# Performance work log

Hardware: AMD Instinct MI355X
Metric: run time of the kernel (lower is better)

## Reference

```python
import jax, jax.numpy as jnp
import numpy as np

B, C_IN, H, W = 8, 32, 64, 64
C = 64  # num_channels


def setup_inputs() -> dict:
    key = jax.random.key(0)
    ks = jax.random.split(key, 9)
    s_in = 1.0 / np.sqrt(C_IN)
    s_c = 1.0 / np.sqrt(C)
    return {
        "x": jax.random.normal(ks[0], (B, C_IN, H, W), dtype=jnp.float32),
        "wq": jax.random.uniform(ks[1], (C, C_IN), jnp.float32, -s_in, s_in),
        "bq": jax.random.uniform(ks[2], (C,), jnp.float32, -s_in, s_in),
        "wk": jax.random.uniform(ks[3], (C, C_IN), jnp.float32, -s_in, s_in),
        "bk": jax.random.uniform(ks[4], (C,), jnp.float32, -s_in, s_in),
        "wv": jax.random.uniform(ks[5], (C, C_IN), jnp.float32, -s_in, s_in),
        "bv": jax.random.uniform(ks[6], (C,), jnp.float32, -s_in, s_in),
        "wo": jax.random.uniform(ks[7], (C_IN, C), jnp.float32, -s_c, s_c),
        "bo": jax.random.uniform(ks[8], (C_IN,), jnp.float32, -s_c, s_c),
    }


def reference(x, wq, bq, wk, bk, wv, bv, wo, bo):
    b, c_in, h, w = x.shape
    n = h * w
    # 1x1 convs == per-pixel linear projections; produce (B, N, C) directly
    q = (jnp.einsum('bchw,oc->bhwo', x, wq) + bq).reshape(b, n, -1)
    k = (jnp.einsum('bchw,oc->bhwo', x, wk) + bk).reshape(b, n, -1)
    v = (jnp.einsum('bchw,oc->bhwo', x, wv) + bv).reshape(b, n, -1)
    # unscaled attention over spatial positions (no 1/sqrt(d) in original)
    scores = jnp.einsum('bnc,bmc->bnm', q, k)  # (B, N, N)
    attn = jax.nn.softmax(scores, axis=-1)
    out = jnp.einsum('bnm,bmc->bnc', attn, v)  # (B, N, C)
    out = out.reshape(b, h, w, -1)
    out = jnp.einsum('bhwc,oc->bohw', out, wo) + bo[None, :, None, None]
    return out + x
```

## Files before the change

kernel.cpp:

```cpp
#include <hip/hip_runtime.h>
#include <hip/hip_bf16.h>

#define CIN    32
#define NPIX   4096
#define DIM    64
#define LOG2E  1.4426950408889634f

#if __has_builtin(__builtin_amdgcn_exp2f)
#define EXP2(x) __builtin_amdgcn_exp2f(x)
#else
#define EXP2(x) exp2f(x)
#endif

typedef float  f32x4  __attribute__((ext_vector_type(4)));
typedef float  f32x16 __attribute__((ext_vector_type(16)));
typedef short  s16x8  __attribute__((ext_vector_type(8)));

#define ZERO16 {0.f,0.f,0.f,0.f,0.f,0.f,0.f,0.f,0.f,0.f,0.f,0.f,0.f,0.f,0.f,0.f}

__device__ __forceinline__ f32x16 mfma32(s16x8 a, s16x8 b, f32x16 c) {
    return __builtin_amdgcn_mfma_f32_32x32x16_bf16(a, b, c, 0, 0, 0);
}


__global__ __launch_bounds__(256) void qkv_proj(
    const float* __restrict__ x,
    const float* __restrict__ wq, const float* __restrict__ bq,
    const float* __restrict__ wk, const float* __restrict__ bk,
    const float* __restrict__ wv, const float* __restrict__ bv,
    __hip_bfloat16* __restrict__ qb, __hip_bfloat16* __restrict__ kb,
    __hip_bfloat16* __restrict__ vb)
{
    __shared__ float Xs[CIN][64];
    __shared__ float wT[3][CIN][DIM];

    const int tid = threadIdx.x;
    const int b   = blockIdx.y;
    const int bx  = blockIdx.x;
    const int n0  = bx * 64;

    for (int i = tid; i < 3 * CIN * DIM; i += 256) {
        int m = i >> 11, r = i & 2047, c = r >> 6, o = r & 63;
        const float* wsrc = (m == 0) ? wq : (m == 1) ? wk : wv;
        float wv0 = wsrc[o * CIN + c];
        wT[m][c][o] = (m == 0) ? wv0 * LOG2E : wv0;
    }
    for (int i = tid * 4; i < CIN * 64; i += 1024) {
        int c = i >> 6, p = i & 63;
        *(f32x4*)&Xs[c][p] = *(const f32x4*)&x[((size_t)b * CIN + c) * NPIX + n0 + p];
    }
    __syncthreads();

    const int w    = tid >> 6;
    const int lane = tid & 63;
    const int l16  = lane >> 2;
    const int quad = lane & 3;

    const int T  = bx * 4 + w;
    const int px = T * 16 + l16;

    float aq[2][8], ak[2][8];
    #pragma unroll
    for (int kb2 = 0; kb2 < 2; kb2++) {
        f32x4 bq0 = *(const f32x4*)&bq[kb2 * 32 + quad * 8];
        f32x4 bq1 = *(const f32x4*)&bq[kb2 * 32 + quad * 8 + 4];
        f32x4 bk0 = *(const f32x4*)&bk[kb2 * 32 + quad * 8];
        f32x4 bk1 = *(const f32x4*)&bk[kb2 * 32 + quad * 8 + 4];
        #pragma unroll
        for (int j = 0; j < 4; j++) {
            aq[kb2][j] = bq0[j] * LOG2E; aq[kb2][j + 4] = bq1[j] * LOG2E;
            ak[kb2][j] = bk0[j];         ak[kb2][j + 4] = bk1[j];
        }
    }
    #pragma unroll 8
    for (int c = 0; c < CIN; c++) {
        const float xc = Xs[c][w * 16 + l16];
        #pragma unroll
        for (int kb2 = 0; kb2 < 2; kb2++) {
            f32x4 q0 = *(const f32x4*)&wT[0][c][kb2 * 32 + quad * 8];
            f32x4 q1 = *(const f32x4*)&wT[0][c][kb2 * 32 + quad * 8 + 4];
            f32x4 k0 = *(const f32x4*)&wT[1][c][kb2 * 32 + quad * 8];
            f32x4 k1 = *(const f32x4*)&wT[1][c][kb2 * 32 + quad * 8 + 4];
            #pragma unroll
            for (int j = 0; j < 4; j++) {
                aq[kb2][j]     += xc * q0[j];
                aq[kb2][j + 4] += xc * q1[j];
                ak[kb2][j]     += xc * k0[j];
                ak[kb2][j + 4] += xc * k1[j];
            }
        }
    }
    {
        const int s   = px >> 5;
        const int key = px & 31;
        #pragma unroll
        for (int kb2 = 0; kb2 < 2; kb2++) {
            union { s16x8 v; __hip_bfloat16 h[8]; } pq, pk;
            #pragma unroll
            for (int j = 0; j < 8; j++) {
                pq.h[j] = __float2bfloat16(aq[kb2][j]);
                pk.h[j] = __float2bfloat16(ak[kb2][j]);
            }
            *(s16x8*)(qb + ((size_t)b * NPIX + px) * DIM + kb2 * 32 + quad * 8) = pq.v;
            const int kt = kb2 * 2 + (quad >> 1);
            const int h  = quad & 1;
            const size_t koff = (size_t)b * 262144
                + ((size_t)(s * 4 + kt) * 64 + h * 32 + key) * 8;
            *(s16x8*)(kb + koff) = pk.v;
        }
    }

    const int ch = w * 16 + l16;
    float av[2][8];
    {
        const float bvc = bv[ch];
        #pragma unroll
        for (int kh = 0; kh < 2; kh++)
            #pragma unroll
            for (int j = 0; j < 8; j++) av[kh][j] = bvc;
    }
    #pragma unroll 8
    for (int c = 0; c < CIN; c++) {
        const float wvc = wT[2][c][ch];
        f32x4 x0 = *(const f32x4*)&Xs[c][quad * 8];
        f32x4 x1 = *(const f32x4*)&Xs[c][quad * 8 + 4];
        f32x4 x2 = *(const f32x4*)&Xs[c][32 + quad * 8];
        f32x4 x3 = *(const f32x4*)&Xs[c][32 + quad * 8 + 4];
        #pragma unroll
        for (int j = 0; j < 4; j++) {
            av[0][j]     += x0[j] * wvc;
            av[0][j + 4] += x1[j] * wvc;
            av[1][j]     += x2[j] * wvc;
            av[1][j + 4] += x3[j] * wvc;
        }
    }
    #pragma unroll
    for (int kh = 0; kh < 2; kh++) {
        const int s = bx * 2 + kh;
        #pragma unroll
        for (int h = 0; h < 2; h++) {
            union { unsigned long long u; __hip_bfloat16 hh[4]; } pv;
            #pragma unroll
            for (int j = 0; j < 4; j++) pv.hh[j] = __float2bfloat16(av[kh][h * 4 + j]);
            const size_t voff = (size_t)b * 262144
                + (size_t)(s * 4 + (ch >> 5) * 2 + (quad >> 1)) * 512
                + (size_t)(h * 32 + (ch & 31)) * 8
                + 4 * (quad & 1);
            *(unsigned long long*)(vb + voff) = pv.u;
        }
    }
}

__global__ __launch_bounds__(512, 2) void attn_fused(
    const __hip_bfloat16* __restrict__ qb,
    const __hip_bfloat16* __restrict__ kbf,
    const __hip_bfloat16* __restrict__ vbf,
    const float* __restrict__ wo, const float* __restrict__ bo,
    const float* __restrict__ x, float* __restrict__ y)
{
    __shared__ __align__(16) char  sm[2][4][4096];
    __shared__ __align__(16) float REDx[4][64][33];
    __shared__ float LRED2[4][32];

    const int tid  = threadIdx.x;
    const int w    = tid >> 6;
    const int g    = w >> 1;
    const int h    = w & 1;
    const int lane = tid & 63;
    const int q    = lane & 31;
    const int hl   = lane >> 5;
    const int b    = blockIdx.x;
    const int row0 = blockIdx.y * 128 + g * 32;

    s16x8 qf[4];
    #pragma unroll
    for (int kt = 0; kt < 4; kt++)
        qf[kt] = *(const s16x8*)(qb + ((size_t)b * NPIX + row0 + q) * DIM
                                 + kt * 16 + hl * 8);

    f32x16 o0 = ZERO16, o1 = ZERO16;
    f32x16 ol = ZERO16;

    s16x8 ones8;
    #pragma unroll
    for (int j = 0; j < 8; j++) ones8[j] = (short)0x3F80;

    const char* stsrc = ((w & 4) ? (const char*)vbf : (const char*)kbf)
                        + (size_t)b * 524288
                        + (size_t)((w >> 1) & 1) * 262144
                        + (size_t)(w & 1) * 2048 + (size_t)lane * 16;
    char* std0 = &sm[0][w >> 1][(w & 1) * 2048 + lane * 16];
    char* std1 = std0 + 16384;

    const char* Kl0 = &sm[0][h][0];
    const char* Vl0 = &sm[0][2 + h][0];

    {
        f32x4 r0 = *(const f32x4*)(stsrc);
        f32x4 r1 = *(const f32x4*)(stsrc + 1024);
        *(f32x4*)(std0)        = r0;
        *(f32x4*)(std0 + 1024) = r1;
    }
    __syncthreads();

    int cur = 0;
    for (int p = 0; p < 64; ++p) {
        const int pn = (p < 63) ? p + 1 : 63;
        f32x4 r0 = *(const f32x4*)(stsrc + (size_t)pn * 4096);
        f32x4 r1 = *(const f32x4*)(stsrc + (size_t)pn * 4096 + 1024);

        const char* Kl = Kl0 + cur * 16384;
        const char* Vl = Vl0 + cur * 16384;
        s16x8 kf[4], cvv[4];
        #pragma unroll
        for (int i = 0; i < 4; i++) kf[i]  = *(const s16x8*)(Kl + i * 1024 + lane * 16);
        #pragma unroll
        for (int i = 0; i < 4; i++) cvv[i] = *(const s16x8*)(Vl + i * 1024 + lane * 16);

        f32x16 sA = ZERO16, sB = ZERO16;
        sA = mfma32(kf[0], qf[0], sA);
        sA = mfma32(kf[1], qf[1], sA);
        sB = mfma32(kf[2], qf[2], sB);
        sB = mfma32(kf[3], qf[3], sB);

        union { s16x8 v; __hip_bfloat16 h8[8]; } p0, p1;
        #pragma unroll
        for (int j = 0; j < 8; j++) {
            p0.h8[j] = __float2bfloat16(EXP2(sA[j] + sB[j]));
            p1.h8[j] = __float2bfloat16(EXP2(sA[8 + j] + sB[8 + j]));
        }

        o0 = mfma32(cvv[0], p0.v, o0);
        o0 = mfma32(cvv[1], p1.v, o0);
        o1 = mfma32(cvv[2], p0.v, o1);
        o1 = mfma32(cvv[3], p1.v, o1);
        ol = mfma32(ones8, p0.v, ol);
        ol = mfma32(ones8, p1.v, ol);

        char* dst = cur ? std0 : std1;
        *(f32x4*)(dst)        = r0;
        *(f32x4*)(dst + 1024) = r1;
        __syncthreads();
        cur ^= 1;
    }

    if (h == 1) {
        #pragma unroll
        for (int i = 0; i < 16; i++) {
            const int rr = (i & 3) + 8 * (i >> 2) + 4 * hl;
            REDx[g][rr][q]      = o0[i];
            REDx[g][32 + rr][q] = o1[i];
        }
        if (hl == 0) LRED2[g][q] = ol[0];
    }
    __syncthreads();

    if (h == 0) {
        const float lsum = ol[0] + LRED2[g][q];
        #pragma unroll
        for (int i = 0; i < 16; i++) {
            const int rr = (i & 3) + 8 * (i >> 2) + 4 * hl;
            o0[i] += REDx[g][rr][q];
            o1[i] += REDx[g][32 + rr][q];
        }
        const float inv = 1.0f / lsum;

        s16x8 pbo[4];
        #pragma unroll
        for (int gg = 0; gg < 4; gg++) {
            union { s16x8 v; __hip_bfloat16 h8[8]; } pk;
            #pragma unroll
            for (int j = 0; j < 8; j++) {
                const float vv = (gg < 2) ? o0[(gg & 1) * 8 + j] : o1[(gg & 1) * 8 + j];
                pk.h8[j] = __float2bfloat16(vv * inv);
            }
            pbo[gg] = pk.v;
        }

        s16x8 aw[4];
        #pragma unroll
        for (int gg = 0; gg < 4; gg++) {
            f32x4 w0 = *(const f32x4*)(wo + (size_t)q * DIM + gg * 16 + hl * 4);
            f32x4 w1 = *(const f32x4*)(wo + (size_t)q * DIM + gg * 16 + 8 + hl * 4);
            union { s16x8 v; __hip_bfloat16 h8[8]; } wf;
            #pragma unroll
            for (int j = 0; j < 4; j++) {
                wf.h8[j]     = __float2bfloat16(w0[j]);
                wf.h8[4 + j] = __float2bfloat16(w1[j]);
            }
            aw[gg] = wf.v;
        }

        f32x16 d = ZERO16;
        #pragma unroll
        for (int gg = 0; gg < 4; gg++)
            d = mfma32(aw[gg], pbo[gg], d);

        #pragma unroll
        for (int i = 0; i < 16; i++) {
            const int out = (i & 3) + 8 * (i >> 2) + 4 * hl;
            const int row = row0 + q;
            const size_t xi = ((size_t)b * CIN + out) * NPIX + row;
            y[xi] = d[i] + bo[out] + x[xi];
        }
    }
}

extern "C" void kernel_launch(void* const* d_in, const int* in_sizes, int n_in,
                              void* d_out, int out_size, void* d_ws, size_t ws_size,
                              hipStream_t stream)
{
    const float* x  = (const float*)d_in[0];
    const float* wq = (const float*)d_in[1];
    const float* bq = (const float*)d_in[2];
    const float* wk = (const float*)d_in[3];
    const float* bk = (const float*)d_in[4];
    const float* wv = (const float*)d_in[5];
    const float* bv = (const float*)d_in[6];
    const float* wo = (const float*)d_in[7];
    const float* bo = (const float*)d_in[8];
    float* y = (float*)d_out;

    char* ws = (char*)d_ws;
    __hip_bfloat16* qb = (__hip_bfloat16*)(ws);
    __hip_bfloat16* kb = (__hip_bfloat16*)(ws + (4u << 20));
    __hip_bfloat16* vb = (__hip_bfloat16*)(ws + (8u << 20));

    qkv_proj<<<dim3(64, 8), dim3(256), 0, stream>>>(x, wq, bq, wk, bk, wv, bv, qb, kb, vb);
    attn_fused<<<dim3(8, 32), dim3(512), 0, stream>>>(qb, kb, vb, wo, bo, x, y);
}
```

Before: 136.8 us.

## Process two key tiles per iteration and compute row sums with scalar adds

Each wave now processes two 32-key tiles per loop iteration, using a double-buffered LDS stage twice as large, so the loop runs half as many iterations and block barriers. The row-sum MFMA with a ones vector is replaced by scalar accumulation of the exponentials plus one cross-lane shuffle, freeing matrix-core cycles. MFMA blocks are wrapped in s_setprio to favour issuing them. The cost is higher register pressure and doubled LDS staging, which may affect occupancy.

```diff
diff --git a/kernel.cpp b/kernel.cpp
--- a/kernel.cpp
+++ b/kernel.cpp
@@ -158,7 +158,7 @@
     const float* __restrict__ wo, const float* __restrict__ bo,
     const float* __restrict__ x, float* __restrict__ y)
 {
-    __shared__ __align__(16) char  sm[2][4][4096];
+    __shared__ __align__(16) char  sm[2][8][4096];
     __shared__ __align__(16) float REDx[4][64][33];
     __shared__ float LRED2[4][32];
 
@@ -179,70 +179,91 @@
                                  + kt * 16 + hl * 8);
 
     f32x16 o0 = ZERO16, o1 = ZERO16;
-    f32x16 ol = ZERO16;
-
-    s16x8 ones8;
+    float lsacc = 0.f;
+
+    const char* stbase = ((w >> 2) ? (const char*)vbf : (const char*)kbf)
+                       + (size_t)b * 524288
+                       + (size_t)((w >> 1) & 1) * 262144
+                       + (size_t)(w & 1) * 4096
+                       + (size_t)lane * 16;
+    char* std0 = &sm[0][w][lane * 16];
+    char* std1 = &sm[1][w][lane * 16];
+
     #pragma unroll
-    for (int j = 0; j < 8; j++) ones8[j] = (short)0x3F80;
-
-    const char* stsrc = ((w & 4) ? (const char*)vbf : (const char*)kbf)
-                        + (size_t)b * 524288
-                        + (size_t)((w >> 1) & 1) * 262144
-                        + (size_t)(w & 1) * 2048 + (size_t)lane * 16;
-    char* std0 = &sm[0][w >> 1][(w & 1) * 2048 + lane * 16];
-    char* std1 = std0 + 16384;
-
-    const char* Kl0 = &sm[0][h][0];
-    const char* Vl0 = &sm[0][2 + h][0];
-
-    {
-        f32x4 r0 = *(const f32x4*)(stsrc);
-        f32x4 r1 = *(const f32x4*)(stsrc + 1024);
-        *(f32x4*)(std0)        = r0;
-        *(f32x4*)(std0 + 1024) = r1;
-    }
+    for (int i = 0; i < 4; i++)
+        *(f32x4*)(std0 + i * 1024) = *(const f32x4*)(stbase + i * 1024);
     __syncthreads();
 
     int cur = 0;
-    for (int p = 0; p < 64; ++p) {
-        const int pn = (p < 63) ? p + 1 : 63;
-        f32x4 r0 = *(const f32x4*)(stsrc + (size_t)pn * 4096);
-        f32x4 r1 = *(const f32x4*)(stsrc + (size_t)pn * 4096 + 1024);
-
-        const char* Kl = Kl0 + cur * 16384;
-        const char* Vl = Vl0 + cur * 16384;
-        s16x8 kf[4], cvv[4];
-        #pragma unroll
-        for (int i = 0; i < 4; i++) kf[i]  = *(const s16x8*)(Kl + i * 1024 + lane * 16);
-        #pragma unroll
-        for (int i = 0; i < 4; i++) cvv[i] = *(const s16x8*)(Vl + i * 1024 + lane * 16);
-
-        f32x16 sA = ZERO16, sB = ZERO16;
-        sA = mfma32(kf[0], qf[0], sA);
-        sA = mfma32(kf[1], qf[1], sA);
-        sB = mfma32(kf[2], qf[2], sB);
-        sB = mfma32(kf[3], qf[3], sB);
-
-        union { s16x8 v; __hip_bfloat16 h8[8]; } p0, p1;
+    for (int p = 0; p < 32; ++p) {
+        const size_t srcoff = (size_t)((p < 31) ? p + 1 : 31) * 8192;
+        f32x4 r0 = *(const f32x4*)(stbase + srcoff);
+        f32x4 r1 = *(const f32x4*)(stbase + srcoff + 1024);
+        f32x4 r2 = *(const f32x4*)(stbase + srcoff + 2048);
+        f32x4 r3 = *(const f32x4*)(stbase + srcoff + 3072);
+
+        const char* K0 = sm[cur][h * 2 + 0];
+        const char* K1 = sm[cur][h * 2 + 1];
+        const char* V0 = sm[cur][4 + h * 2 + 0];
+        const char* V1 = sm[cur][4 + h * 2 + 1];
+        s16x8 kf0[4], kf1[4], vv0[4], vv1[4];
+        #pragma unroll
+        for (int i = 0; i < 4; i++) {
+            kf0[i] = *(const s16x8*)(K0 + i * 1024 + lane * 16);
+            kf1[i] = *(const s16x8*)(K1 + i * 1024 + lane * 16);
+            vv0[i] = *(const s16x8*)(V0 + i * 1024 + lane * 16);
+            vv1[i] = *(const s16x8*)(V1 + i * 1024 + lane * 16);
+        }
+
+        __builtin_amdgcn_s_setprio(1);
+        f32x16 s0 = ZERO16, s1 = ZERO16;
+        s0 = mfma32(kf0[0], qf[0], s0);
+        s1 = mfma32(kf1[0], qf[0], s1);
+        s0 = mfma32(kf0[1], qf[1], s0);
+        s1 = mfma32(kf1[1], qf[1], s1);
+        s0 = mfma32(kf0[2], qf[2], s0);
+        s1 = mfma32(kf1[2], qf[2], s1);
+        s0 = mfma32(kf0[3], qf[3], s0);
+        s1 = mfma32(kf1[3], qf[3], s1);
+        __builtin_amdgcn_s_setprio(0);
+
+        union { s16x8 v; __hip_bfloat16 h8[8]; } p00, p01, p10, p11;
+        #pragma unroll
+        for (int r = 0; r < 16; r++) { s0[r] = EXP2(s0[r]); lsacc += s0[r]; }
         #pragma unroll
         for (int j = 0; j < 8; j++) {
-            p0.h8[j] = __float2bfloat16(EXP2(sA[j] + sB[j]));
-            p1.h8[j] = __float2bfloat16(EXP2(sA[8 + j] + sB[8 + j]));
-        }
-
-        o0 = mfma32(cvv[0], p0.v, o0);
-        o0 = mfma32(cvv[1], p1.v, o0);
-        o1 = mfma32(cvv[2], p0.v, o1);
-        o1 = mfma32(cvv[3], p1.v, o1);
-        ol = mfma32(ones8, p0.v, ol);
-        ol = mfma32(ones8, p1.v, ol);
+            p00.h8[j] = __float2bfloat16(s0[j]);
+            p01.h8[j] = __float2bfloat16(s0[8 + j]);
+        }
+        #pragma unroll
+        for (int r = 0; r < 16; r++) { s1[r] = EXP2(s1[r]); lsacc += s1[r]; }
+        #pragma unroll
+        for (int j = 0; j < 8; j++) {
+            p10.h8[j] = __float2bfloat16(s1[j]);
+            p11.h8[j] = __float2bfloat16(s1[8 + j]);
+        }
+
+        __builtin_amdgcn_s_setprio(1);
+        o0 = mfma32(vv0[0], p00.v, o0);
+        o1 = mfma32(vv0[2], p00.v, o1);
+        o0 = mfma32(vv0[1], p01.v, o0);
+        o1 = mfma32(vv0[3], p01.v, o1);
+        o0 = mfma32(vv1[0], p10.v, o0);
+        o1 = mfma32(vv1[2], p10.v, o1);
+        o0 = mfma32(vv1[1], p11.v, o0);
+        o1 = mfma32(vv1[3], p11.v, o1);
+        __builtin_amdgcn_s_setprio(0);
 
         char* dst = cur ? std0 : std1;
         *(f32x4*)(dst)        = r0;
         *(f32x4*)(dst + 1024) = r1;
+        *(f32x4*)(dst + 2048) = r2;
+        *(f32x4*)(dst + 3072) = r3;
         __syncthreads();
         cur ^= 1;
     }
+
+    lsacc += __shfl_xor(lsacc, 32, 64);
 
     if (h == 1) {
         #pragma unroll
@@ -251,12 +272,12 @@
             REDx[g][rr][q]      = o0[i];
             REDx[g][32 + rr][q] = o1[i];
         }
-        if (hl == 0) LRED2[g][q] = ol[0];
+        if (hl == 0) LRED2[g][q] = lsacc;
     }
     __syncthreads();
 
     if (h == 0) {
-        const float lsum = ol[0] + LRED2[g][q];
+        const float lsum = lsacc + LRED2[g][q];
         #pragma unroll
         for (int i = 0; i < 16; i++) {
             const int rr = (i & 3) + 8 * (i >> 2) + 4 * hl;
```

Result: faster. 127.6 us (-6.7%).
